# Kernel tuning notes

Hardware: AMD Instinct MI355X
Metric: run time of the kernel (lower is better)

## Reference

```python
import jax, jax.numpy as jnp
import numpy as np
import math

N_NODES = 16384
N_GRAPHS = 512
E2 = 65536
E3 = 393216
EMB = 300
SCH = 128
NG = 50
CUTOFF = 10.0
NL_GIN = 5
NL_SCH = 6
NTASK = 12


def _ssp(x):
    # ShiftedSoftplus used by SchNet
    return jax.nn.softplus(x) - math.log(2.0)


def _seg(x, ids, n):
    return jax.ops.segment_sum(x, ids, num_segments=n)


def _forward(x2d, edge_index_2d, edge_attr_2d, batch, z, pos, edge_index_3d,
             atom_emb1, atom_emb2, vn_init,
             gin_W1, gin_b1, gin_W2, gin_b2, gin_bond1, gin_bond2, gin_gamma, gin_beta,
             vn_W1, vn_b1, vn_W2, vn_b2,
             sch_emb, s_mW1, s_mb1, s_mW2, s_mb2, s_lin1W, s_lin2W, s_lin2b, s_linW, s_linb,
             p2W, p2b, p3W, p3b, gW1, gb1, gW2, gb2, cW1, cb1, cW2, cb2):
    counts = jnp.maximum(_seg(jnp.ones((N_NODES,), jnp.float32), batch, N_GRAPHS), 1.0)[:, None]
    # ---------- GIN (2D) encoder with virtual node (OGB-style, eval mode: dropout off, BN uses running stats 0/1) ----------
    src2, dst2 = edge_index_2d[0], edge_index_2d[1]
    h = atom_emb1[x2d[:, 0]] + atom_emb2[x2d[:, 1]]              # [N, 300]
    vn = jnp.broadcast_to(vn_init, (N_GRAPHS, EMB))
    for l in range(NL_GIN):
        h_in = h + vn[batch]
        eemb = gin_bond1[l][edge_attr_2d[:, 0]] + gin_bond2[l][edge_attr_2d[:, 1]]
        msg = jax.nn.relu(h_in[src2] + eemb)                     # [E2, 300]
        agg = _seg(msg, dst2, N_NODES)
        t = jax.nn.relu((h_in + agg) @ gin_W1[l] + gin_b1[l]) @ gin_W2[l] + gin_b2[l]
        t = t * gin_gamma[l] + gin_beta[l]                       # eval-mode BatchNorm
        if l < NL_GIN - 1:
            t = jax.nn.relu(t)
            vn_tmp = _seg(t, batch, N_GRAPHS) + vn
            vn = jax.nn.relu(jax.nn.relu(vn_tmp @ vn_W1[l] + vn_b1[l]) @ vn_W2[l] + vn_b2[l])
        h = t
    h2d = _seg(h, batch, N_GRAPHS) / counts                      # global_mean_pool
    # ---------- SchNet (3D) encoder: interaction layers only, residual additions ----------
    src3, dst3 = edge_index_3d[0], edge_index_3d[1]
    diff = pos[dst3] - pos[src3]
    d = jnp.sqrt(jnp.sum(diff * diff, axis=-1))                  # edge_weight [E3]; no self loops -> d > 0
    offsets = jnp.linspace(0.0, CUTOFF, NG)
    coeff = -0.5 / (offsets[1] - offsets[0]) ** 2
    rbf = jnp.exp(coeff * (d[:, None] - offsets) ** 2)           # GaussianSmearing [E3, 50]
    C = 0.5 * (jnp.cos(d * math.pi / CUTOFF) + 1.0)              # cosine cutoff
    hs = sch_emb[z]                                              # [N, 128]
    for l in range(NL_SCH):
        Wf = (_ssp(rbf @ s_mW1[l] + s_mb1[l]) @ s_mW2[l] + s_mb2[l]) * C[:, None]  # filter net [E3, 128]
        x1 = hs @ s_lin1W[l]                                     # CFConv lin1 (no bias)
        agg = _seg(x1[src3] * Wf, dst3, N_NODES)                 # continuous-filter conv
        x2 = agg @ s_lin2W[l] + s_lin2b[l]                       # CFConv lin2
        hs = hs + (_ssp(x2) @ s_linW[l] + s_linb[l])             # block act+lin, residual
    h3d = _seg(hs, batch, N_GRAPHS) / counts
    # ---------- gated fusion + classifier (dropout off in eval) ----------
    h2p = h2d @ p2W + p2b
    h3p = h3d @ p3W + p3b
    g = jax.nn.sigmoid(jax.nn.relu(jnp.concatenate([h2p, h3p], axis=1) @ gW1 + gb1) @ gW2 + gb2)  # [B, 1]
    hf = g * h2p + (1.0 - g) * h3p
    return jax.nn.relu(hf @ cW1 + cb1) @ cW2 + cb2               # [N_GRAPHS, NTASK]


def setup_inputs() -> dict:
    key = jax.random.key(0)
    ks = jax.random.split(key, 40)
    def r(i, shape, s=0.02):
        return jax.random.normal(ks[i], shape, dtype=jnp.float32) * s
    x2d = jax.random.randint(ks[0], (N_NODES, 2), 0, 3)
    src2 = jax.random.randint(ks[1], (E2,), 0, N_NODES)
    dst2 = (src2 + jax.random.randint(ks[2], (E2,), 1, N_NODES)) % N_NODES  # no self loops
    edge_index_2d = jnp.stack([src2, dst2])
    edge_attr_2d = jax.random.randint(ks[3], (E2, 2), 0, 3)
    batch = jnp.sort(jax.random.randint(ks[4], (N_NODES,), 0, N_GRAPHS))
    z = jax.random.randint(ks[5], (N_NODES,), 0, 100)
    pos = jax.random.normal(ks[6], (N_NODES, 3), dtype=jnp.float32) * 2.0
    src3 = jax.random.randint(ks[7], (E3,), 0, N_NODES)
    dst3 = (src3 + jax.random.randint(ks[8], (E3,), 1, N_NODES)) % N_NODES
    edge_index_3d = jnp.stack([src3, dst3])
    return dict(
        x2d=x2d, edge_index_2d=edge_index_2d, edge_attr_2d=edge_attr_2d, batch=batch,
        z=z, pos=pos, edge_index_3d=edge_index_3d,
        atom_emb1=r(9, (120, EMB)), atom_emb2=r(10, (3, EMB)),
        vn_init=jnp.zeros((EMB,), jnp.float32),
        gin_W1=r(11, (NL_GIN, EMB, 2 * EMB)), gin_b1=jnp.zeros((NL_GIN, 2 * EMB), jnp.float32),
        gin_W2=r(12, (NL_GIN, 2 * EMB, EMB)), gin_b2=jnp.zeros((NL_GIN, EMB), jnp.float32),
        gin_bond1=r(13, (NL_GIN, 6, EMB)), gin_bond2=r(14, (NL_GIN, 3, EMB)),
        gin_gamma=jnp.ones((NL_GIN, EMB), jnp.float32), gin_beta=jnp.zeros((NL_GIN, EMB), jnp.float32),
        vn_W1=r(15, (NL_GIN - 1, EMB, 2 * EMB)), vn_b1=jnp.zeros((NL_GIN - 1, 2 * EMB), jnp.float32),
        vn_W2=r(16, (NL_GIN - 1, 2 * EMB, EMB)), vn_b2=jnp.zeros((NL_GIN - 1, EMB), jnp.float32),
        sch_emb=r(17, (100, SCH), 0.1),
        s_mW1=r(18, (NL_SCH, NG, SCH), 0.1), s_mb1=jnp.zeros((NL_SCH, SCH), jnp.float32),
        s_mW2=r(19, (NL_SCH, SCH, SCH), 0.1), s_mb2=jnp.zeros((NL_SCH, SCH), jnp.float32),
        s_lin1W=r(20, (NL_SCH, SCH, SCH), 0.1),
        s_lin2W=r(21, (NL_SCH, SCH, SCH), 0.1), s_lin2b=jnp.zeros((NL_SCH, SCH), jnp.float32),
        s_linW=r(22, (NL_SCH, SCH, SCH), 0.1), s_linb=jnp.zeros((NL_SCH, SCH), jnp.float32),
        p2W=r(23, (EMB, EMB)), p2b=jnp.zeros((EMB,), jnp.float32),
        p3W=r(24, (SCH, EMB)), p3b=jnp.zeros((EMB,), jnp.float32),
        gW1=r(25, (2 * EMB, 128)), gb1=jnp.zeros((128,), jnp.float32),
        gW2=r(26, (128, 1)), gb2=jnp.zeros((1,), jnp.float32),
        cW1=r(27, (EMB, EMB // 2)), cb1=jnp.zeros((EMB // 2,), jnp.float32),
        cW2=r(28, (EMB // 2, NTASK)), cb2=jnp.zeros((NTASK,), jnp.float32),
    )


def reference(x2d, edge_index_2d, edge_attr_2d, batch, z, pos, edge_index_3d,
              atom_emb1, atom_emb2, vn_init,
              gin_W1, gin_b1, gin_W2, gin_b2, gin_bond1, gin_bond2, gin_gamma, gin_beta,
              vn_W1, vn_b1, vn_W2, vn_b2,
              sch_emb, s_mW1, s_mb1, s_mW2, s_mb2, s_lin1W, s_lin2W, s_lin2b, s_linW, s_linb,
              p2W, p2b, p3W, p3b, gW1, gb1, gW2, gb2, cW1, cb1, cW2, cb2):
    return _forward(x2d, edge_index_2d, edge_attr_2d, batch, z, pos, edge_index_3d,
                    atom_emb1, atom_emb2, vn_init,
                    gin_W1, gin_b1, gin_W2, gin_b2, gin_bond1, gin_bond2, gin_gamma, gin_beta,
                    vn_W1, vn_b1, vn_W2, vn_b2,
                    sch_emb, s_mW1, s_mb1, s_mW2, s_mb2, s_lin1W, s_lin2W, s_lin2b, s_linW, s_linb,
                    p2W, p2b, p3W, p3b, gW1, gb1, gW2, gb2, cW1, cb1, cW2, cb2)
```

## Files before the change

### kernel.cpp

```cpp
#include <hip/hip_runtime.h>
#include <hip/hip_bf16.h>
#include <math.h>

#define NN 16384
#define NG 512
#define NE2 65536
#define NE3 393216
#define DEMB 300
#define DSCH 128
#define NRBF 50
#define NTAB 5120
#define TROWS 5121
#define DMAX 25.0f

typedef __attribute__((ext_vector_type(8))) short bf16x8;
typedef __attribute__((ext_vector_type(4))) float f32x4;

__device__ __forceinline__ float sspf(float x) {
  float sp = log1pf(expf(-fabsf(x))) + fmaxf(x, 0.f);
  return sp - 0.69314718055994530942f;
}

__device__ __forceinline__ short f2b(float f) {
  union { float f; unsigned u; } v;
  v.f = f;
  unsigned r = v.u + 0x7FFF + ((v.u >> 16) & 1);
  return (short)(r >> 16);
}

__device__ __forceinline__ float b2f(unsigned short b) {
  union { unsigned u; float f; } v;
  v.u = ((unsigned)b) << 16;
  return v.f;
}

__device__ __forceinline__ unsigned pk2(float a, float b) {
  return ((unsigned)(unsigned short)f2b(b) << 16) | (unsigned short)f2b(a);
}


__global__ void k_hist3(const int* __restrict__ ei2, const int* __restrict__ ei3,
                        const int* __restrict__ batch, int* __restrict__ cnt2,
                        int* __restrict__ cnt3, int* __restrict__ cntg) {
  int i = blockIdx.x * blockDim.x + threadIdx.x;
  if (i < NE2) {
    atomicAdd(&cnt2[ei2[NE2 + i]], 1);
  } else if (i < NE2 + NE3) {
    atomicAdd(&cnt3[ei3[NE3 + (i - NE2)]], 1);
  } else if (i < NE2 + NE3 + NN) {
    atomicAdd(&cntg[batch[i - NE2 - NE3]], 1);
  }
}

__global__ __launch_bounds__(1024) void k_scan3(const int* __restrict__ c0, int* __restrict__ o0,
                                                int n0, const int* __restrict__ c1,
                                                int* __restrict__ o1, int n1,
                                                const int* __restrict__ c2, int* __restrict__ o2,
                                                int n2) {
  const int* cnt = (blockIdx.x == 0) ? c0 : (blockIdx.x == 1) ? c1 : c2;
  int* off = (blockIdx.x == 0) ? o0 : (blockIdx.x == 1) ? o1 : o2;
  int n = (blockIdx.x == 0) ? n0 : (blockIdx.x == 1) ? n1 : n2;
  __shared__ int part[1024];
  int tid = threadIdx.x;
  int per = (n + 1023) / 1024;
  int base = tid * per;
  int sum = 0;
  for (int i = 0; i < per; ++i) {
    int idx = base + i;
    if (idx < n) sum += cnt[idx];
  }
  part[tid] = sum;
  __syncthreads();
  for (int d = 1; d < 1024; d <<= 1) {
    int v = (tid >= d) ? part[tid - d] : 0;
    __syncthreads();
    part[tid] += v;
    __syncthreads();
  }
  int run = (tid == 0) ? 0 : part[tid - 1];
  for (int i = 0; i < per; ++i) {
    int idx = base + i;
    if (idx < n) {
      off[idx] = run;
      run += cnt[idx];
    }
  }
  if (tid == 0) off[n] = part[1023];
}

__global__ void k_scatterB(const int* __restrict__ ei2, const int* __restrict__ ea2,
                           const int* __restrict__ batch, const int* __restrict__ off2,
                           int* __restrict__ cur2, int4* __restrict__ em2,
                           const int* __restrict__ ei3, const float* __restrict__ pos,
                           const int* __restrict__ off3, int* __restrict__ cur3,
                           int4* __restrict__ em3) {
  int i = blockIdx.x * blockDim.x + threadIdx.x;
  if (i < NE2) {
    int e = i;
    int s = ei2[e], d = ei2[NE2 + e];
    int p = atomicAdd(&cur2[d], 1);
    int j = off2[d] + p;
    em2[j] = make_int4(s, ea2[2 * e] * 4 + ea2[2 * e + 1], batch[s], 0);
  } else if (i < NE2 + NE3) {
    int e = i - NE2;
    int s = ei3[e], d = ei3[NE3 + e];
    float dx = pos[3 * d] - pos[3 * s];
    float dy = pos[3 * d + 1] - pos[3 * s + 1];
    float dz = pos[3 * d + 2] - pos[3 * s + 2];
    float dist = sqrtf(dx * dx + dy * dy + dz * dz);
    float u = fminf(dist * ((float)NTAB / DMAX), (float)NTAB - 0.001f);
    int idx = (int)u;
    int p = atomicAdd(&cur3[d], 1);
    int j = off3[d] + p;
    em3[j] = make_int4(s, idx, __float_as_int(u - (float)idx), 0);
  }
}


__global__ void k_init_gin(const int* __restrict__ x2d, const float* __restrict__ e1,
                           const float* __restrict__ e2, short* __restrict__ hb,
                           const float* __restrict__ vni, float* __restrict__ vn,
                           short* __restrict__ vnb) {
  int i = blockIdx.x * blockDim.x + threadIdx.x;
  if (i < NN * DEMB) {
    int n = i / DEMB, c = i - n * DEMB;
    hb[i] = f2b(e1[x2d[2 * n] * DEMB + c] + e2[x2d[2 * n + 1] * DEMB + c]);
  } else if (i < NN * DEMB + NG * DEMB) {
    int j = i - NN * DEMB;
    float v = vni[j % DEMB];
    vn[j] = v;
    vnb[j] = f2b(v);
  }
}

__global__ void k_init_sch(float* __restrict__ rbs, float* __restrict__ Cs,
                           const int* __restrict__ z, const float* __restrict__ emb,
                           float* __restrict__ hs, short* __restrict__ hsb) {
  int i = blockIdx.x * blockDim.x + threadIdx.x;
  if (i < TROWS * NRBF) {
    int j = i / NRBF, k = i - j * NRBF;
    float dj = (float)j * (DMAX / (float)NTAB);
    const float step = 10.0f / 49.0f;
    const float coeff = -0.5f / (step * step);
    float t = dj - (float)k * step;
    rbs[i] = expf(coeff * t * t);
    if (k == 0) Cs[j] = 0.5f * (cosf(dj * (3.14159265358979323846f / 10.0f)) + 1.0f);
  } else if (i < TROWS * NRBF + NN * DSCH) {
    int j = i - TROWS * NRBF;
    float v = emb[z[j >> 7] * DSCH + (j & 127)];
    hs[j] = v;
    hsb[j] = f2b(v);
  }
}


__device__ __forceinline__ void gin_edge_add(const unsigned* __restrict__ hr,
                                             const unsigned* __restrict__ vr,
                                             const unsigned* __restrict__ eu, int u0, int u1,
                                             int u2, bool has2, float* acc) {
  unsigned a = hr[u0], b = vr[u0], e = eu[u0];
  acc[0] += fmaxf(b2f((unsigned short)a) + b2f((unsigned short)b) + b2f((unsigned short)e), 0.f);
  acc[1] += fmaxf(b2f((unsigned short)(a >> 16)) + b2f((unsigned short)(b >> 16)) +
                      b2f((unsigned short)(e >> 16)), 0.f);
  a = hr[u1]; b = vr[u1]; e = eu[u1];
  acc[2] += fmaxf(b2f((unsigned short)a) + b2f((unsigned short)b) + b2f((unsigned short)e), 0.f);
  acc[3] += fmaxf(b2f((unsigned short)(a >> 16)) + b2f((unsigned short)(b >> 16)) +
                      b2f((unsigned short)(e >> 16)), 0.f);
  if (has2) {
    a = hr[u2]; b = vr[u2]; e = eu[u2];
    acc[4] += fmaxf(b2f((unsigned short)a) + b2f((unsigned short)b) + b2f((unsigned short)e), 0.f);
    acc[5] += fmaxf(b2f((unsigned short)(a >> 16)) + b2f((unsigned short)(b >> 16)) +
                        b2f((unsigned short)(e >> 16)), 0.f);
  }
}

__global__ __launch_bounds__(256) void k_gin_gather6(
    const short* __restrict__ hb, const short* __restrict__ vnb, const int* __restrict__ batch,
    const int* __restrict__ off2, const int4* __restrict__ em2, const float* __restrict__ bond1,
    const float* __restrict__ bond2, short* __restrict__ aggb) {
  __shared__ unsigned sb[18 * 150];
  int tid = threadIdx.x;
  for (int i = tid; i < 18 * 150; i += 256) {
    int c = i / 150, u = i - c * 150;
    int a0 = c / 3, a1 = c - a0 * 3;
    float v0 = bond1[a0 * 300 + 2 * u] + bond2[a1 * 300 + 2 * u];
    float v1 = bond1[a0 * 300 + 2 * u + 1] + bond2[a1 * 300 + 2 * u + 1];
    sb[i] = pk2(v0, v1);
  }
  __syncthreads();
  int d = blockIdx.x * 4 + (tid >> 6);
  int l = tid & 63;
  int j0 = off2[d], j1 = off2[d + 1];
  const unsigned* hu = (const unsigned*)hb + (size_t)d * 150;
  const unsigned* vu = (const unsigned*)vnb + (size_t)batch[d] * 150;
  const int u0 = l, u1 = l + 64, u2 = l + 128;
  const bool has2 = (u2 < 150);
  float acc[6];
  {
    unsigned a = hu[u0], b = vu[u0];
    acc[0] = b2f((unsigned short)a) + b2f((unsigned short)b);
    acc[1] = b2f((unsigned short)(a >> 16)) + b2f((unsigned short)(b >> 16));
    a = hu[u1]; b = vu[u1];
    acc[2] = b2f((unsigned short)a) + b2f((unsigned short)b);
    acc[3] = b2f((unsigned short)(a >> 16)) + b2f((unsigned short)(b >> 16));
    if (has2) {
      a = hu[u2]; b = vu[u2];
      acc[4] = b2f((unsigned short)a) + b2f((unsigned short)b);
      acc[5] = b2f((unsigned short)(a >> 16)) + b2f((unsigned short)(b >> 16));
    } else {
      acc[4] = acc[5] = 0.f;
    }
  }
  int j = j0;
  for (; j + 1 < j1; j += 2) {
    int4 mA = em2[j], mB = em2[j + 1];
    const unsigned* hrA = (const unsigned*)hb + (size_t)mA.x * 150;
    const unsigned* vrA = (const unsigned*)vnb + (size_t)mA.z * 150;
    const unsigned* euA = sb + ((mA.y >> 2) * 3 + (mA.y & 3)) * 150;
    const unsigned* hrB = (const unsigned*)hb + (size_t)mB.x * 150;
    const unsigned* vrB = (const unsigned*)vnb + (size_t)mB.z * 150;
    const unsigned* euB = sb + ((mB.y >> 2) * 3 + (mB.y & 3)) * 150;
    gin_edge_add(hrA, vrA, euA, u0, u1, u2, has2, acc);
    gin_edge_add(hrB, vrB, euB, u0, u1, u2, has2, acc);
  }
  if (j < j1) {
    int4 m = em2[j];
    gin_edge_add((const unsigned*)hb + (size_t)m.x * 150, (const unsigned*)vnb + (size_t)m.z * 150,
                 sb + ((m.y >> 2) * 3 + (m.y & 3)) * 150, u0, u1, u2, has2, acc);
  }
  unsigned* outu = (unsigned*)aggb + (size_t)d * 160;
  outu[u0] = pk2(acc[0], acc[1]);
  outu[u1] = pk2(acc[2], acc[3]);
  if (u2 < 160) outu[u2] = has2 ? pk2(acc[4], acc[5]) : 0u;
}

__global__ __launch_bounds__(256) void k_conv_gather6(
    const short* __restrict__ ftabb, const short* __restrict__ x1b, const int* __restrict__ off3,
    const int4* __restrict__ em3, short* __restrict__ agg3b) {
  __shared__ float2 sm[2][64];
  int tid = threadIdx.x;
  int slot = tid >> 7;
  int wh = (tid >> 6) & 1;
  int lane = tid & 63;
  int d = blockIdx.x * 2 + slot;
  int j0 = off3[d], j1 = off3[d + 1];
  int mid = j0 + ((j1 - j0 + 1) >> 1);
  int jb = wh ? mid : j0;
  int je = wh ? j1 : mid;
  float a0 = 0.f, a1 = 0.f;
  int j = jb;
  for (; j + 1 < je; j += 2) {
    int4 mA = em3[j], mB = em3[j + 1];
    float frA = __int_as_float(mA.z), frB = __int_as_float(mB.z);
    unsigned t0A = ((const unsigned*)(ftabb + (size_t)mA.y * 128))[lane];
    unsigned t1A = ((const unsigned*)(ftabb + (size_t)(mA.y + 1) * 128))[lane];
    unsigned xvA = ((const unsigned*)(x1b + (size_t)mA.x * 128))[lane];
    unsigned t0B = ((const unsigned*)(ftabb + (size_t)mB.y * 128))[lane];
    unsigned t1B = ((const unsigned*)(ftabb + (size_t)(mB.y + 1) * 128))[lane];
    unsigned xvB = ((const unsigned*)(x1b + (size_t)mB.x * 128))[lane];
    {
      float t0a = b2f((unsigned short)t0A), t0b = b2f((unsigned short)(t0A >> 16));
      float t1a = b2f((unsigned short)t1A), t1b = b2f((unsigned short)(t1A >> 16));
      a0 += (t0a + frA * (t1a - t0a)) * b2f((unsigned short)(xvA & 0xFFFF));
      a1 += (t0b + frA * (t1b - t0b)) * b2f((unsigned short)(xvA >> 16));
    }
    {
      float t0a = b2f((unsigned short)t0B), t0b = b2f((unsigned short)(t0B >> 16));
      float t1a = b2f((unsigned short)t1B), t1b = b2f((unsigned short)(t1B >> 16));
      a0 += (t0a + frB * (t1a - t0a)) * b2f((unsigned short)(xvB & 0xFFFF));
      a1 += (t0b + frB * (t1b - t0b)) * b2f((unsigned short)(xvB >> 16));
    }
  }
  if (j < je) {
    int4 m = em3[j];
    float fr = __int_as_float(m.z);
    unsigned t0 = ((const unsigned*)(ftabb + (size_t)m.y * 128))[lane];
    unsigned t1 = ((const unsigned*)(ftabb + (size_t)(m.y + 1) * 128))[lane];
    unsigned xv = ((const unsigned*)(x1b + (size_t)m.x * 128))[lane];
    float t0a = b2f((unsigned short)t0), t0b = b2f((unsigned short)(t0 >> 16));
    float t1a = b2f((unsigned short)t1), t1b = b2f((unsigned short)(t1 >> 16));
    a0 += (t0a + fr * (t1a - t0a)) * b2f((unsigned short)(xv & 0xFFFF));
    a1 += (t0b + fr * (t1b - t0b)) * b2f((unsigned short)(xv >> 16));
  }
  if (wh == 1) sm[slot][lane] = make_float2(a0, a1);
  __syncthreads();
  if (wh == 0) {
    float2 p = sm[slot][lane];
    ((unsigned*)(agg3b + (size_t)d * 128))[lane] = pk2(a0 + p.x, a1 + p.y);
  }
}

__global__ __launch_bounds__(256) void k_poolvn(const short* __restrict__ hb,
                                                const int* __restrict__ goff,
                                                const float* __restrict__ vn,
                                                short* __restrict__ vnab) {
  int g = blockIdx.x * 4 + (threadIdx.x >> 6);
  int l = threadIdx.x & 63;
  if (g >= NG) return;
  int r0 = goff[g], r1 = goff[g + 1];
  const int u0 = l, u1 = l + 64, u2 = l + 128;
  const bool has2 = (u2 < 150);
  float acc[6] = {};
  for (int r = r0; r < r1; ++r) {
    const unsigned* hu = (const unsigned*)hb + (size_t)r * 150;
    unsigned a = hu[u0];
    acc[0] += b2f((unsigned short)a);
    acc[1] += b2f((unsigned short)(a >> 16));
    a = hu[u1];
    acc[2] += b2f((unsigned short)a);
    acc[3] += b2f((unsigned short)(a >> 16));
    if (has2) {
      a = hu[u2];
      acc[4] += b2f((unsigned short)a);
      acc[5] += b2f((unsigned short)(a >> 16));
    }
  }
  const float2* v2 = (const float2*)(vn + (size_t)g * 300);
  unsigned* outu = (unsigned*)vnab + (size_t)g * 160;
  float2 w = v2[u0];
  outu[u0] = pk2(acc[0] + w.x, acc[1] + w.y);
  w = v2[u1];
  outu[u1] = pk2(acc[2] + w.x, acc[3] + w.y);
  if (u2 < 160) {
    if (has2) {
      w = v2[u2];
      outu[u2] = pk2(acc[4] + w.x, acc[5] + w.y);
    } else {
      outu[u2] = 0u;
    }
  }
}

__global__ __launch_bounds__(256) void k_poolhead2(const short* __restrict__ hb,
                                                   const int* __restrict__ goff,
                                                   short* __restrict__ xcat) {
  int g = blockIdx.x * 4 + (threadIdx.x >> 6);
  int l = threadIdx.x & 63;
  if (g >= NG) return;
  int r0 = goff[g], r1 = goff[g + 1];
  const int u0 = l, u1 = l + 64, u2 = l + 128;
  const bool has2 = (u2 < 150);
  float acc[6] = {};
  for (int r = r0; r < r1; ++r) {
    const unsigned* hu = (const unsigned*)hb + (size_t)r * 150;
    unsigned a = hu[u0];
    acc[0] += b2f((unsigned short)a);
    acc[1] += b2f((unsigned short)(a >> 16));
    a = hu[u1];
    acc[2] += b2f((unsigned short)a);
    acc[3] += b2f((unsigned short)(a >> 16));
    if (has2) {
      a = hu[u2];
      acc[4] += b2f((unsigned short)a);
      acc[5] += b2f((unsigned short)(a >> 16));
    }
  }
  float s = 1.0f / fmaxf((float)(r1 - r0), 1.0f);
  unsigned* outu = (unsigned*)xcat + (size_t)g * 224;
  outu[u0] = pk2(acc[0] * s, acc[1] * s);
  outu[u1] = pk2(acc[2] * s, acc[3] * s);
  if (u2 < 160) outu[u2] = has2 ? pk2(acc[4] * s, acc[5] * s) : 0u;
}

__global__ __launch_bounds__(256) void k_poolhead3(const short* __restrict__ hsb,
                                                   const int* __restrict__ goff,
                                                   short* __restrict__ xcat) {
  int g = blockIdx.x * 4 + (threadIdx.x >> 6);
  int l = threadIdx.x & 63;
  if (g >= NG) return;
  int r0 = goff[g], r1 = goff[g + 1];
  float a0 = 0.f, a1 = 0.f;
  for (int r = r0; r < r1; ++r) {
    unsigned v = ((const unsigned*)hsb)[(size_t)r * 64 + l];
    a0 += b2f((unsigned short)(v & 0xFFFF));
    a1 += b2f((unsigned short)(v >> 16));
  }
  float s = 1.0f / fmaxf((float)(r1 - r0), 1.0f);
  ((unsigned*)xcat)[(size_t)g * 224 + 160 + l] = pk2(a0 * s, a1 * s);
}

__global__ __launch_bounds__(256) void k_blend(const float* __restrict__ gh,
                                               const float* __restrict__ gW2,
                                               const float* __restrict__ gb2,
                                               const float* __restrict__ hcat,
                                               short* __restrict__ hfb) {
  int g = blockIdx.x * 4 + (threadIdx.x >> 6);
  int l = threadIdx.x & 63;
  if (g >= NG) return;
  float2 v = ((const float2*)(gh + (size_t)g * 128))[l];
  float dot = v.x * gW2[2 * l] + v.y * gW2[2 * l + 1];
  for (int m = 32; m; m >>= 1) dot += __shfl_xor(dot, m);
  float gg = 1.0f / (1.0f + expf(-(dot + gb2[0])));
  const float* hc = hcat + (size_t)g * 608;
  unsigned* outu = (unsigned*)hfb + (size_t)g * 160;
  const int u0 = l, u1 = l + 64, u2 = l + 128;
  float a0 = hc[2 * u0], a1 = hc[2 * u0 + 1], b0 = hc[304 + 2 * u0], b1 = hc[304 + 2 * u0 + 1];
  outu[u0] = pk2(gg * a0 + (1.f - gg) * b0, gg * a1 + (1.f - gg) * b1);
  a0 = hc[2 * u1]; a1 = hc[2 * u1 + 1]; b0 = hc[304 + 2 * u1]; b1 = hc[304 + 2 * u1 + 1];
  outu[u1] = pk2(gg * a0 + (1.f - gg) * b0, gg * a1 + (1.f - gg) * b1);
  if (u2 < 160) {
    if (u2 < 150) {
      a0 = hc[2 * u2]; a1 = hc[2 * u2 + 1]; b0 = hc[304 + 2 * u2]; b1 = hc[304 + 2 * u2 + 1];
      outu[u2] = pk2(gg * a0 + (1.f - gg) * b0, gg * a1 + (1.f - gg) * b1);
    } else {
      outu[u2] = 0u;
    }
  }
}

__global__ void k_prepw2(const float* __restrict__ Wa, const float* __restrict__ Wb,
                         short* __restrict__ Wta, short* __restrict__ Wtb, int K, int N, int Kp,
                         int Np, int La, int Lb) {
  int i = blockIdx.x * blockDim.x + threadIdx.x;
  int per = Np * Kp;
  if (i >= (La + Lb) * per) return;
  int l = i / per, r = i - l * per;
  int n = r / Kp, k = r - n * Kp;
  const float* W = (l < La) ? Wa : Wb;
  int ll = (l < La) ? l : l - La;
  short* Wt = (l < La) ? Wta : Wtb;
  float v = (n < N && k < K) ? W[(size_t)ll * K * N + (size_t)k * N + n] : 0.f;
  Wt[(size_t)ll * per + r] = f2b(v);
}

__global__ void k_prepw3(const float* __restrict__ W0, const float* __restrict__ W1,
                         const float* __restrict__ W2, short* __restrict__ T0,
                         short* __restrict__ T1, short* __restrict__ T2) {
  int i = blockIdx.x * blockDim.x + threadIdx.x;
  const int per = 6 * 128 * 128;
  if (i >= 3 * per) return;
  int which = i / per, r = i - which * per;
  int l = r / 16384, rr = r - l * 16384;
  int n = rr / 128, k = rr - n * 128;
  const float* W = (which == 0) ? W0 : (which == 1) ? W1 : W2;
  short* T = (which == 0) ? T0 : (which == 1) ? T1 : T2;
  T[r] = f2b(W[(size_t)l * 16384 + (size_t)k * 128 + n]);
}

#define W1SZ (608 * 448)
#define G1SZ (128 * 608)
#define C1SZ (160 * 320)
#define C2SZ (12 * 160)
__global__ void k_prephead(const float* __restrict__ p2W, const float* __restrict__ p2b,
                           const float* __restrict__ p3W, const float* __restrict__ p3b,
                           const float* __restrict__ gW1, const float* __restrict__ cW1,
                           const float* __restrict__ cb1, const float* __restrict__ cW2,
                           short* __restrict__ Wcat, short* __restrict__ gW1cat,
                           short* __restrict__ cW1cat, short* __restrict__ cW2cat,
                           float* __restrict__ bcat, float* __restrict__ cb1p) {
  int i = blockIdx.x * blockDim.x + threadIdx.x;
  if (i < W1SZ) {
    int o = i / 448, k = i - o * 448;
    float v = 0.f;
    if (o < 300 && k < 300) v = p2W[(size_t)k * 300 + o];
    else if (o >= 304 && o < 604 && k >= 320) v = p3W[(size_t)(k - 320) * 300 + (o - 304)];
    Wcat[i] = f2b(v);
  } else if (i < W1SZ + G1SZ) {
    int r = i - W1SZ;
    int o = r / 608, k = r - o * 608;
    float v = 0.f;
    if (k < 300) v = gW1[(size_t)k * 128 + o];
    else if (k >= 304 && k < 604) v = gW1[(size_t)(300 + k - 304) * 128 + o];
    gW1cat[r] = f2b(v);
  } else if (i < W1SZ + G1SZ + C1SZ) {
    int r = i - W1SZ - G1SZ;
    int o = r / 320, k = r - o * 320;
    cW1cat[r] = f2b((o < 150 && k < 300) ? cW1[(size_t)k * 150 + o] : 0.f);
  } else if (i < W1SZ + G1SZ + C1SZ + C2SZ) {
    int r = i - W1SZ - G1SZ - C1SZ;
    int o = r / 160, k = r - o * 160;
    cW2cat[r] = f2b((k < 150) ? cW2[(size_t)k * 12 + o] : 0.f);
  } else if (i < W1SZ + G1SZ + C1SZ + C2SZ + 608) {
    int o = i - W1SZ - G1SZ - C1SZ - C2SZ;
    bcat[o] = (o < 300) ? p2b[o] : (o >= 304 && o < 604) ? p3b[o - 304] : 0.f;
  } else if (i < W1SZ + G1SZ + C1SZ + C2SZ + 608 + 160) {
    int o = i - W1SZ - G1SZ - C1SZ - C2SZ - 608;
    cb1p[o] = (o < 150) ? cb1[o] : 0.f;
  }
}

template <int ACT>
__global__ __launch_bounds__(256) void k_gemmz(
    const float* __restrict__ A, const float* __restrict__ B, const float* __restrict__ bias,
    const float* __restrict__ rscale, float* __restrict__ Cout, short* __restrict__ Coutb,
    int M, int N, int K, int ldc, long strideA, long strideB, long strideBias, long strideC) {
  A += (size_t)blockIdx.z * strideA;
  B += (size_t)blockIdx.z * strideB;
  bias += (size_t)blockIdx.z * strideBias;
  __shared__ float sA[16][65];
  __shared__ float sB[16][64];
  int tid = threadIdx.x;
  int tx = tid & 15, ty = tid >> 4;
  int bm = blockIdx.y * 64, bn = blockIdx.x * 64;
  float acc[4][4] = {};
  for (int k0 = 0; k0 < K; k0 += 16) {
#pragma unroll
    for (int t = 0; t < 4; ++t) {
      int i = tid + t * 256;
      int m = i >> 4, kk = i & 15;
      int gm = bm + m, gk = k0 + kk;
      sA[kk][m] = (gm < M && gk < K) ? A[(size_t)gm * K + gk] : 0.f;
    }
#pragma unroll
    for (int t = 0; t < 4; ++t) {
      int i = tid + t * 256;
      int kk = i >> 6, n = i & 63;
      int gk = k0 + kk, gn = bn + n;
      sB[kk][n] = (gk < K && gn < N) ? B[(size_t)gk * N + gn] : 0.f;
    }
    __syncthreads();
#pragma unroll
    for (int kk = 0; kk < 16; ++kk) {
      float a[4], b[4];
#pragma unroll
      for (int i = 0; i < 4; ++i) a[i] = sA[kk][ty + 16 * i];
#pragma unroll
      for (int j = 0; j < 4; ++j) b[j] = sB[kk][tx + 16 * j];
#pragma unroll
      for (int i = 0; i < 4; ++i)
#pragma unroll
        for (int j = 0; j < 4; ++j) acc[i][j] = fmaf(a[i], b[j], acc[i][j]);
    }
    __syncthreads();
  }
#pragma unroll
  for (int i = 0; i < 4; ++i) {
    int gm = bm + ty + 16 * i;
    if (gm >= M) continue;
    float rs = rscale ? rscale[gm] : 1.0f;
#pragma unroll
    for (int j = 0; j < 4; ++j) {
      int gn = bn + tx + 16 * j;
      if (gn >= N) continue;
      float v = acc[i][j] + bias[gn];
      if (ACT == 1) v = fmaxf(v, 0.f);
      if (ACT == 2) v = sspf(v);
      v *= rs;
      if (Cout) Cout[(size_t)blockIdx.z * strideC + (size_t)gm * ldc + gn] = v;
      if (Coutb) Coutb[(size_t)blockIdx.z * strideC + (size_t)gm * ldc + gn] = f2b(v);
    }
  }
}

template <int ACT>
__global__ __launch_bounds__(256) void k_mgemm_bf64(
    const short* __restrict__ Ab, const short* __restrict__ Wt, const float* __restrict__ bias,
    const float* __restrict__ scale, const float* __restrict__ shift,
    const float* __restrict__ Cin, float* __restrict__ Cout, short* __restrict__ Coutb,
    int M, int N, int Kp, int ldc, int ldcb, int Nb) {
  __shared__ short sA[64 * 32];
  const int tid = threadIdx.x;
  const int lane = tid & 63;
  const int w = tid >> 6;
  const int bm = blockIdx.y * 64, bn = blockIdx.x * 128;

  f32x4 acc[4][2] = {};

  const int sr = tid >> 2;
  const int sk = (tid & 3) * 8;
  const short* Arow = Ab + (size_t)(bm + sr) * Kp + sk;
  const int ssw = (sr + (sr >> 2)) & 3;
  const int s0 = tid & 3;
  bf16x8* sAv = (bf16x8*)sA;

  const int frow = lane & 15;
  const int fslot = lane >> 4;
  const short* Bbase = Wt + (size_t)(bn + w * 32 + (lane & 15)) * Kp + (fslot * 8);

  for (int k0 = 0; k0 < Kp; k0 += 32) {
    __syncthreads();
    sAv[sr * 4 + (s0 ^ ssw)] = *(const bf16x8*)(Arow + k0);
    __syncthreads();

    bf16x8 af[4], bfr[2];
#pragma unroll
    for (int mf = 0; mf < 4; ++mf) {
      int r = frow + mf * 16;
      af[mf] = sAv[r * 4 + (fslot ^ ((r + (r >> 2)) & 3))];
    }
#pragma unroll
    for (int nf = 0; nf < 2; ++nf) bfr[nf] = *(const bf16x8*)(Bbase + (size_t)nf * 16 * Kp + k0);
#pragma unroll
    for (int mf = 0; mf < 4; ++mf)
#pragma unroll
      for (int nf = 0; nf < 2; ++nf)
        acc[mf][nf] =
            __builtin_amdgcn_mfma_f32_16x16x32_bf16(af[mf], bfr[nf], acc[mf][nf], 0, 0, 0);
  }

  const int colbase = bn + w * 32 + (lane & 15);
  const int rowbase = bm + ((lane >> 4) << 2);
#pragma unroll
  for (int nf = 0; nf < 2; ++nf) {
    int col = colbase + nf * 16;
    bool cv = col < N;
    float bi = (bias && cv) ? bias[col] : 0.f;
    float sc = (scale && cv) ? scale[col] : 1.f;
    float sh = (shift && cv) ? shift[col] : 0.f;
#pragma unroll
    for (int mf = 0; mf < 4; ++mf) {
      f32x4 v = acc[mf][nf];
#pragma unroll
      for (int j = 0; j < 4; ++j) {
        int row = rowbase + mf * 16 + j;
        float x = v[j] + bi;
        if (scale) x = x * sc + sh;
        if (ACT == 1) x = fmaxf(x, 0.f);
        if (ACT == 2) x = sspf(x);
        if (Cin && cv) x += Cin[(size_t)row * ldc + col];
        if (Cout && cv) Cout[(size_t)row * ldc + col] = x;
        if (Coutb && col < Nb) Coutb[(size_t)row * ldcb + col] = cv ? f2b(x) : (short)0;
      }
    }
  }
}

template <int LAST>
__global__ __launch_bounds__(256) void k_sch_fused(
    const short* __restrict__ agg3b, const short* __restrict__ W2t, const float* __restrict__ b2,
    const short* __restrict__ W3t, const float* __restrict__ b3, const short* __restrict__ W1n,
    float* __restrict__ hs, short* __restrict__ hsb, short* __restrict__ x1b) {
  __shared__ short sA[64 * 128];
  __shared__ short sY[64 * 128];
  const int tid = threadIdx.x;
  const int lane = tid & 63;
  const int w = tid >> 6;
  const int bm = blockIdx.x * 64;
  bf16x8* sAv = (bf16x8*)sA;
  bf16x8* sYv = (bf16x8*)sY;
  {
    int r = tid >> 2, q = tid & 3;
    int ssw = (r + (r >> 2)) & 3;
    const short* Arow = agg3b + (size_t)(bm + r) * 128 + q * 8;
#pragma unroll
    for (int c = 0; c < 4; ++c) sAv[r * 16 + c * 4 + (q ^ ssw)] = *(const bf16x8*)(Arow + c * 32);
  }
  __syncthreads();
  const int frow = lane & 15;
  const int fslot = lane >> 4;
  const int colw = w * 32 + (lane & 15);
  const int rw0 = (lane >> 4) << 2;
  {
    f32x4 acc[4][2] = {};
    const short* Bbase = W2t + (size_t)colw * 128 + fslot * 8;
#pragma unroll
    for (int c = 0; c < 4; ++c) {
      bf16x8 af[4], bfr[2];
#pragma unroll
      for (int mf = 0; mf < 4; ++mf) {
        int r = frow + mf * 16;
        af[mf] = sAv[r * 16 + c * 4 + (fslot ^ ((r + (r >> 2)) & 3))];
      }
#pragma unroll
      for (int nf = 0; nf < 2; ++nf) bfr[nf] = *(const bf16x8*)(Bbase + nf * 16 * 128 + c * 32);
#pragma unroll
      for (int mf = 0; mf < 4; ++mf)
#pragma unroll
        for (int nf = 0; nf < 2; ++nf)
          acc[mf][nf] =
              __builtin_amdgcn_mfma_f32_16x16x32_bf16(af[mf], bfr[nf], acc[mf][nf], 0, 0, 0);
    }
#pragma unroll
    for (int nf = 0; nf < 2; ++nf) {
      int cl = colw + nf * 16;
      float bi = b2[cl];
#pragma unroll
      for (int mf = 0; mf < 4; ++mf)
#pragma unroll
        for (int j = 0; j < 4; ++j) {
          int rw = rw0 + mf * 16 + j;
          float y = sspf(acc[mf][nf][j] + bi);
          int slot = (cl >> 5) * 4 + (((cl >> 3) & 3) ^ ((rw + (rw >> 2)) & 3));
          sY[rw * 128 + slot * 8 + (cl & 7)] = f2b(y);
        }
    }
  }
  __syncthreads();
  {
    f32x4 acc[4][2] = {};
    const short* Bbase = W3t + (size_t)colw * 128 + fslot * 8;
#pragma unroll
    for (int c = 0; c < 4; ++c) {
      bf16x8 af[4], bfr[2];
#pragma unroll
      for (int mf = 0; mf < 4; ++mf) {
        int r = frow + mf * 16;
        af[mf] = sYv[r * 16 + c * 4 + (fslot ^ ((r + (r >> 2)) & 3))];
      }
#pragma unroll
      for (int nf = 0; nf < 2; ++nf) bfr[nf] = *(const bf16x8*)(Bbase + nf * 16 * 128 + c * 32);
#pragma unroll
      for (int mf = 0; mf < 4; ++mf)
#pragma unroll
        for (int nf = 0; nf < 2; ++nf)
          acc[mf][nf] =
              __builtin_amdgcn_mfma_f32_16x16x32_bf16(af[mf], bfr[nf], acc[mf][nf], 0, 0, 0);
    }
#pragma unroll
    for (int nf = 0; nf < 2; ++nf) {
      int cl = colw + nf * 16;
      float bi = b3[cl];
#pragma unroll
      for (int mf = 0; mf < 4; ++mf)
#pragma unroll
        for (int j = 0; j < 4; ++j) {
          int rw = rw0 + mf * 16 + j;
          size_t gi = (size_t)(bm + rw) * 128 + cl;
          float x = acc[mf][nf][j] + bi + hs[gi];
          hs[gi] = x;
          short xb = f2b(x);
          hsb[gi] = xb;
          int slot = (cl >> 5) * 4 + (((cl >> 3) & 3) ^ ((rw + (rw >> 2)) & 3));
          sA[rw * 128 + slot * 8 + (cl & 7)] = xb;
        }
    }
  }
  if (LAST) return;
  __syncthreads();
  {
    f32x4 acc[4][2] = {};
    const short* Bbase = W1n + (size_t)colw * 128 + fslot * 8;
#pragma unroll
    for (int c = 0; c < 4; ++c) {
      bf16x8 af[4], bfr[2];
#pragma unroll
      for (int mf = 0; mf < 4; ++mf) {
        int r = frow + mf * 16;
        af[mf] = sAv[r * 16 + c * 4 + (fslot ^ ((r + (r >> 2)) & 3))];
      }
#pragma unroll
      for (int nf = 0; nf < 2; ++nf) bfr[nf] = *(const bf16x8*)(Bbase + nf * 16 * 128 + c * 32);
#pragma unroll
      for (int mf = 0; mf < 4; ++mf)
#pragma unroll
        for (int nf = 0; nf < 2; ++nf)
          acc[mf][nf] =
              __builtin_amdgcn_mfma_f32_16x16x32_bf16(af[mf], bfr[nf], acc[mf][nf], 0, 0, 0);
    }
#pragma unroll
    for (int nf = 0; nf < 2; ++nf) {
      int cl = colw + nf * 16;
#pragma unroll
      for (int mf = 0; mf < 4; ++mf)
#pragma unroll
        for (int j = 0; j < 4; ++j) {
          int rw = rw0 + mf * 16 + j;
          x1b[(size_t)(bm + rw) * 128 + cl] = f2b(acc[mf][nf][j]);
        }
    }
  }
}


static inline void run_mgemm_bf64(hipStream_t st, const short* Ab, const short* Wt,
                                  const float* bias, const float* scale, const float* shift,
                                  const float* Cin, float* Cout, short* Coutb, int M, int N,
                                  int Kp, int ldc, int ldcb, int Nb, int act) {
  dim3 grid((N + 127) / 128, M / 64);
  if (act == 0)
    k_mgemm_bf64<0><<<grid, 256, 0, st>>>(Ab, Wt, bias, scale, shift, Cin, Cout, Coutb, M, N, Kp,
                                          ldc, ldcb, Nb);
  else if (act == 1)
    k_mgemm_bf64<1><<<grid, 256, 0, st>>>(Ab, Wt, bias, scale, shift, Cin, Cout, Coutb, M, N, Kp,
                                          ldc, ldcb, Nb);
  else
    k_mgemm_bf64<2><<<grid, 256, 0, st>>>(Ab, Wt, bias, scale, shift, Cin, Cout, Coutb, M, N, Kp,
                                          ldc, ldcb, Nb);
}

extern "C" void kernel_launch(void* const* d_in, const int* in_sizes, int n_in, void* d_out,
                              int out_size, void* d_ws, size_t ws_size, hipStream_t stream) {
  const int* x2d = (const int*)d_in[0];
  const int* ei2 = (const int*)d_in[1];
  const int* ea2 = (const int*)d_in[2];
  const int* batch = (const int*)d_in[3];
  const int* z = (const int*)d_in[4];
  const float* pos = (const float*)d_in[5];
  const int* ei3 = (const int*)d_in[6];
  const float* atom_emb1 = (const float*)d_in[7];
  const float* atom_emb2 = (const float*)d_in[8];
  const float* vn_init = (const float*)d_in[9];
  const float* gin_W1 = (const float*)d_in[10];
  const float* gin_b1 = (const float*)d_in[11];
  const float* gin_W2 = (const float*)d_in[12];
  const float* gin_b2 = (const float*)d_in[13];
  const float* gin_bond1 = (const float*)d_in[14];
  const float* gin_bond2 = (const float*)d_in[15];
  const float* gin_gamma = (const float*)d_in[16];
  const float* gin_beta = (const float*)d_in[17];
  const float* vn_W1 = (const float*)d_in[18];
  const float* vn_b1 = (const float*)d_in[19];
  const float* vn_W2 = (const float*)d_in[20];
  const float* vn_b2 = (const float*)d_in[21];
  const float* sch_emb = (const float*)d_in[22];
  const float* s_mW1 = (const float*)d_in[23];
  const float* s_mb1 = (const float*)d_in[24];
  const float* s_mW2 = (const float*)d_in[25];
  const float* s_mb2 = (const float*)d_in[26];
  const float* s_lin1W = (const float*)d_in[27];
  const float* s_lin2W = (const float*)d_in[28];
  const float* s_lin2b = (const float*)d_in[29];
  const float* s_linW = (const float*)d_in[30];
  const float* s_linb = (const float*)d_in[31];
  const float* p2W = (const float*)d_in[32];
  const float* p2b = (const float*)d_in[33];
  const float* p3W = (const float*)d_in[34];
  const float* p3b = (const float*)d_in[35];
  const float* gW1 = (const float*)d_in[36];
  const float* gb1 = (const float*)d_in[37];
  const float* gW2 = (const float*)d_in[38];
  const float* gb2 = (const float*)d_in[39];
  const float* cW1 = (const float*)d_in[40];
  const float* cb1 = (const float*)d_in[41];
  const float* cW2 = (const float*)d_in[42];
  const float* cb2 = (const float*)d_in[43];

  float* ws = (float*)d_ws;
  short* hb = (short*)ws;
  short* aggb = (short*)(ws + 5000000);
  short* y1b = (short*)(ws + 7700000);
  float* rbs = ws + 400000;
  float* Cs = ws + 700000;
  float* t1all = ws + 800000;
  short* ftabb = (short*)(ws + 4800000);
  float* hs = ws + 8800000;
  short* x1b = (short*)(ws + 11000000);
  short* agg3b = (short*)(ws + 13200000);
  short* hsb = (short*)(ws + 15400000);
  short* W1t = (short*)(ws + 20000000);
  short* W2t = (short*)(ws + 20600000);
  short* s1t = (short*)(ws + 21200000);
  short* s2t = (short*)(ws + 21300000);
  short* s3t = (short*)(ws + 21400000);
  int* I = (int*)(ws + 22000000);
  int* cnt2 = I + 0;
  int* cnt3 = I + 16384;
  int* cntg = I + 32768;
  int* cur2 = I + 33280;
  int* cur3 = I + 49664;
  int* off2 = I + 70000;
  int* off3 = I + 90000;
  int* goff = I + 110000;
  int4* em2 = (int4*)(I + 120000);
  int4* em3 = (int4*)(I + 400000);
  short* vnW1t = (short*)(ws + 24000000);
  short* vnW2t = (short*)(ws + 24420000);
  short* vnab = (short*)(ws + 24900000);
  short* vnhb = (short*)(ws + 24990000);
  short* vnb = (short*)(ws + 25150000);
  short* Wcat = (short*)(ws + 25300000);
  short* gW1cat = (short*)(ws + 25440000);
  short* cW1cat = (short*)(ws + 25480000);
  short* cW2cat = (short*)(ws + 25510000);
  float* bcat = ws + 25520000;
  float* cb1p = ws + 25521000;
  short* xcat = (short*)(ws + 25530000);
  float* hcat = ws + 25650000;
  short* hcatb = (short*)(ws + 25970000);
  float* gh = ws + 26130000;
  short* hfb = (short*)(ws + 26200000);
  short* c1b = (short*)(ws + 26290000);
  float* vn = ws + 28443136;

  k_prepw2<<<(9 * 640 * 320 + 255) / 256, 256, 0, stream>>>(gin_W1, vn_W1, W1t, vnW1t, 300, 600,
                                                            320, 640, 5, 4);
  k_prepw2<<<(9 * 384 * 608 + 255) / 256, 256, 0, stream>>>(gin_W2, vn_W2, W2t, vnW2t, 600, 300,
                                                            608, 384, 5, 4);
  k_prepw3<<<(3 * 6 * 16384 + 255) / 256, 256, 0, stream>>>(s_lin1W, s_lin2W, s_linW, s1t, s2t,
                                                            s3t);
  k_prephead<<<(W1SZ + G1SZ + C1SZ + C2SZ + 608 + 160 + 255) / 256, 256, 0, stream>>>(
      p2W, p2b, p3W, p3b, gW1, cW1, cb1, cW2, Wcat, gW1cat, cW1cat, cW2cat, bcat, cb1p);

  hipMemsetAsync(I, 0, 66048 * sizeof(int), stream);
  k_hist3<<<(NE2 + NE3 + NN + 255) / 256, 256, 0, stream>>>(ei2, ei3, batch, cnt2, cnt3, cntg);
  k_scan3<<<3, 1024, 0, stream>>>(cnt2, off2, 16384, cnt3, off3, 16384, cntg, goff, 512);
  k_scatterB<<<(NE2 + NE3 + 255) / 256, 256, 0, stream>>>(ei2, ea2, batch, off2, cur2, em2, ei3,
                                                          pos, off3, cur3, em3);

  k_init_gin<<<(NN * DEMB + NG * DEMB + 255) / 256, 256, 0, stream>>>(x2d, atom_emb1, atom_emb2,
                                                                      hb, vn_init, vn, vnb);
  for (int l = 0; l < 5; ++l) {
    k_gin_gather6<<<NN / 4, 256, 0, stream>>>(hb, vnb, batch, off2, em2,
                                              gin_bond1 + l * 6 * DEMB, gin_bond2 + l * 3 * DEMB,
                                              aggb);
    run_mgemm_bf64(stream, aggb, W1t + (size_t)l * 640 * 320, gin_b1 + l * 600, nullptr, nullptr,
                   nullptr, nullptr, y1b, NN, 600, 320, 0, 608, 608, 1);
    run_mgemm_bf64(stream, y1b, W2t + (size_t)l * 384 * 608, gin_b2 + l * 300,
                   gin_gamma + l * 300, gin_beta + l * 300, nullptr, nullptr, hb, NN, 300, 608, 0,
                   300, 300, (l < 4) ? 1 : 0);
    if (l < 4) {
      k_poolvn<<<NG / 4, 256, 0, stream>>>(hb, goff, vn, vnab);
      run_mgemm_bf64(stream, vnab, vnW1t + (size_t)l * 640 * 320, vn_b1 + l * 600, nullptr,
                     nullptr, nullptr, nullptr, vnhb, NG, 600, 320, 0, 608, 608, 1);
      run_mgemm_bf64(stream, vnhb, vnW2t + (size_t)l * 384 * 608, vn_b2 + l * 300, nullptr,
                     nullptr, nullptr, vn, vnb, NG, 300, 608, 300, 300, 300, 1);
    }
  }
  k_poolhead2<<<NG / 4, 256, 0, stream>>>(hb, goff, xcat);

  k_init_sch<<<(TROWS * NRBF + NN * DSCH + 255) / 256, 256, 0, stream>>>(rbs, Cs, z, sch_emb, hs,
                                                                         hsb);
  {
    dim3 ga(2, (TROWS + 63) / 64, 6);
    k_gemmz<2><<<ga, 256, 0, stream>>>(rbs, s_mW1, s_mb1, nullptr, t1all, nullptr, TROWS, 128, 50,
                                       128, 0L, 50L * 128, 128L, (long)TROWS * 128);
    k_gemmz<0><<<ga, 256, 0, stream>>>(t1all, s_mW2, s_mb2, Cs, nullptr, ftabb, TROWS, 128, 128,
                                       128, (long)TROWS * 128, 128L * 128, 128L,
                                       (long)TROWS * 128);
  }
  run_mgemm_bf64(stream, hsb, s1t, nullptr, nullptr, nullptr, nullptr, nullptr, x1b, NN, 128, 128,
                 0, 128, 128, 0);
  for (int l = 0; l < 6; ++l) {
    k_conv_gather6<<<NN / 2, 256, 0, stream>>>(ftabb + (size_t)l * TROWS * 128, x1b, off3, em3,
                                               agg3b);
    if (l < 5)
      k_sch_fused<0><<<NN / 64, 256, 0, stream>>>(agg3b, s2t + (size_t)l * 16384,
                                                  s_lin2b + l * 128, s3t + (size_t)l * 16384,
                                                  s_linb + l * 128, s1t + (size_t)(l + 1) * 16384,
                                                  hs, hsb, x1b);
    else
      k_sch_fused<1><<<NN / 64, 256, 0, stream>>>(agg3b, s2t + (size_t)l * 16384,
                                                  s_lin2b + l * 128, s3t + (size_t)l * 16384,
                                                  s_linb + l * 128, s1t, hs, hsb, x1b);
  }
  k_poolhead3<<<NG / 4, 256, 0, stream>>>(hsb, goff, xcat);

  run_mgemm_bf64(stream, xcat, Wcat, bcat, nullptr, nullptr, nullptr, hcat, hcatb, NG, 608, 448,
                 608, 608, 608, 0);
  run_mgemm_bf64(stream, hcatb, gW1cat, gb1, nullptr, nullptr, nullptr, gh, nullptr, NG, 128, 608,
                 128, 128, 0, 1);
  k_blend<<<NG / 4, 256, 0, stream>>>(gh, gW2, gb2, hcat, hfb);
  run_mgemm_bf64(stream, hfb, cW1cat, cb1p, nullptr, nullptr, nullptr, nullptr, c1b, NG, 160, 320,
                 0, 160, 160, 1);
  run_mgemm_bf64(stream, c1b, cW2cat, cb2, nullptr, nullptr, nullptr, (float*)d_out, nullptr, NG,
                 12, 160, 12, 12, 0, 0);
}
```

Before: 1.190 ms.

## Fuse GIN two-layer MLP GEMMs into one kernel keeping hidden tile in LDS

Replaces the two separate bf16 MFMA GEMM launches of each GIN layer's MLP with one kernel. Each block handles 32 rows: it stages the aggregated input in shared memory, computes the 600-wide ReLU hidden layer into a swizzled LDS buffer, then runs the second GEMM with bias, BatchNorm affine and optional ReLU, writing bf16 h. This avoids writing and re-reading the 16384x608 intermediate in global memory and saves one launch per layer. In exchange, weight fragments are read directly from global/L2 with no LDS tiling, the 32-row tiles give less weight reuse per block, and the ~52KB LDS footprint may limit occupancy.

```diff
diff --git a/kernel.cpp b/kernel.cpp
--- a/kernel.cpp
+++ b/kernel.cpp
@@ -610,6 +610,105 @@
         if (Cin && cv) x += Cin[(size_t)row * ldc + col];
         if (Cout && cv) Cout[(size_t)row * ldc + col] = x;
         if (Coutb && col < Nb) Coutb[(size_t)row * ldcb + col] = cv ? f2b(x) : (short)0;
+      }
+    }
+  }
+}
+
+template <int ACT>
+__global__ __launch_bounds__(256) void k_gin_fused(
+    const short* __restrict__ aggb, const short* __restrict__ W1t, const float* __restrict__ b1,
+    const short* __restrict__ W2t, const float* __restrict__ b2, const float* __restrict__ gamma,
+    const float* __restrict__ beta, short* __restrict__ hb) {
+  __shared__ short sA[32 * 320];
+  __shared__ short sY[32 * 640];
+  const int tid = threadIdx.x;
+  const int lane = tid & 63;
+  const int w = tid >> 6;
+  const int bm = blockIdx.x * 32;
+  bf16x8* sAv = (bf16x8*)sA;
+  bf16x8* sYv = (bf16x8*)sY;
+  {
+    int r = tid >> 3, q8 = tid & 7;
+    int ssw = (r + (r >> 2)) & 3;
+    const short* Arow = aggb + (size_t)(bm + r) * 320;
+#pragma unroll
+    for (int jj = 0; jj < 5; ++jj) {
+      int s = q8 + jj * 8;
+      int c = s >> 2, q = s & 3;
+      sAv[r * 40 + c * 4 + (q ^ ssw)] = *(const bf16x8*)(Arow + s * 8);
+    }
+  }
+  __syncthreads();
+  const int frow = lane & 15;
+  const int fslot = lane >> 4;
+  const int rw0 = (lane >> 4) << 2;
+  {
+    f32x4 acc[2][10] = {};
+#pragma unroll
+    for (int c = 0; c < 10; ++c) {
+      bf16x8 af[2];
+#pragma unroll
+      for (int mf = 0; mf < 2; ++mf) {
+        int r = frow + mf * 16;
+        af[mf] = sAv[r * 40 + c * 4 + (fslot ^ ((r + (r >> 2)) & 3))];
+      }
+#pragma unroll
+      for (int nf = 0; nf < 10; ++nf) {
+        bf16x8 bfr = *(const bf16x8*)(W1t + (size_t)(w * 160 + nf * 16 + frow) * 320 +
+                                      fslot * 8 + c * 32);
+        acc[0][nf] = __builtin_amdgcn_mfma_f32_16x16x32_bf16(af[0], bfr, acc[0][nf], 0, 0, 0);
+        acc[1][nf] = __builtin_amdgcn_mfma_f32_16x16x32_bf16(af[1], bfr, acc[1][nf], 0, 0, 0);
+      }
+    }
+#pragma unroll
+    for (int nf = 0; nf < 10; ++nf) {
+      int cl = w * 160 + nf * 16 + frow;
+      float bi = (cl < 600) ? b1[cl] : 0.f;
+#pragma unroll
+      for (int mf = 0; mf < 2; ++mf)
+#pragma unroll
+        for (int j = 0; j < 4; ++j) {
+          int rw = rw0 + mf * 16 + j;
+          float y = fmaxf(acc[mf][nf][j] + bi, 0.f);
+          int s = cl >> 3, c2 = s >> 2, q2 = s & 3;
+          sY[rw * 640 + (c2 * 4 + (q2 ^ ((rw + (rw >> 2)) & 3))) * 8 + (cl & 7)] = f2b(y);
+        }
+    }
+  }
+  __syncthreads();
+  {
+    f32x4 acc[2][6] = {};
+#pragma unroll
+    for (int c = 0; c < 19; ++c) {
+      bf16x8 af[2];
+#pragma unroll
+      for (int mf = 0; mf < 2; ++mf) {
+        int r = frow + mf * 16;
+        af[mf] = sYv[r * 80 + c * 4 + (fslot ^ ((r + (r >> 2)) & 3))];
+      }
+#pragma unroll
+      for (int nf = 0; nf < 6; ++nf) {
+        bf16x8 bfr = *(const bf16x8*)(W2t + (size_t)(w * 96 + nf * 16 + frow) * 608 +
+                                      fslot * 8 + c * 32);
+        acc[0][nf] = __builtin_amdgcn_mfma_f32_16x16x32_bf16(af[0], bfr, acc[0][nf], 0, 0, 0);
+        acc[1][nf] = __builtin_amdgcn_mfma_f32_16x16x32_bf16(af[1], bfr, acc[1][nf], 0, 0, 0);
+      }
+    }
+#pragma unroll
+    for (int nf = 0; nf < 6; ++nf) {
+      int cl = w * 96 + nf * 16 + frow;
+      if (cl < 300) {
+        float bi = b2[cl], sc = gamma[cl], sh = beta[cl];
+#pragma unroll
+        for (int mf = 0; mf < 2; ++mf)
+#pragma unroll
+          for (int j = 0; j < 4; ++j) {
+            int rw = rw0 + mf * 16 + j;
+            float x = (acc[mf][nf][j] + bi) * sc + sh;
+            if (ACT) x = fmaxf(x, 0.f);
+            hb[(size_t)(bm + rw) * 300 + cl] = f2b(x);
+          }
       }
     }
   }
@@ -818,7 +917,6 @@
   float* ws = (float*)d_ws;
   short* hb = (short*)ws;
   short* aggb = (short*)(ws + 5000000);
-  short* y1b = (short*)(ws + 7700000);
   float* rbs = ws + 400000;
   float* Cs = ws + 700000;
   float* t1all = ws + 800000;
@@ -883,11 +981,16 @@
     k_gin_gather6<<<NN / 4, 256, 0, stream>>>(hb, vnb, batch, off2, em2,
                                               gin_bond1 + l * 6 * DEMB, gin_bond2 + l * 3 * DEMB,
                                               aggb);
-    run_mgemm_bf64(stream, aggb, W1t + (size_t)l * 640 * 320, gin_b1 + l * 600, nullptr, nullptr,
-                   nullptr, nullptr, y1b, NN, 600, 320, 0, 608, 608, 1);
-    run_mgemm_bf64(stream, y1b, W2t + (size_t)l * 384 * 608, gin_b2 + l * 300,
-                   gin_gamma + l * 300, gin_beta + l * 300, nullptr, nullptr, hb, NN, 300, 608, 0,
-                   300, 300, (l < 4) ? 1 : 0);
+    if (l < 4)
+      k_gin_fused<1><<<NN / 32, 256, 0, stream>>>(aggb, W1t + (size_t)l * 640 * 320,
+                                                  gin_b1 + l * 600, W2t + (size_t)l * 384 * 608,
+                                                  gin_b2 + l * 300, gin_gamma + l * 300,
+                                                  gin_beta + l * 300, hb);
+    else
+      k_gin_fused<0><<<NN / 32, 256, 0, stream>>>(aggb, W1t + (size_t)l * 640 * 320,
+                                                  gin_b1 + l * 600, W2t + (size_t)l * 384 * 608,
+                                                  gin_b2 + l * 300, gin_gamma + l * 300,
+                                                  gin_beta + l * 300, hb);
     if (l < 4) {
       k_poolvn<<<NG / 4, 256, 0, stream>>>(hb, goff, vn, vnab);
       run_mgemm_bf64(stream, vnab, vnW1t + (size_t)l * 640 * 320, vn_b1 + l * 600, nullptr,
```

New measurement: 1.211 ms. Within noise of the previous version (+1.8%).
